# Kernel optimization log

Measured on AMD Instinct MI355X. Metric: run time of the kernel, lower is better.

The kernel has to match this reference:

```python
import jax, jax.numpy as jnp
import numpy as np

D = 256          # B == num_experts == hidden_dim == input_dim (required by the module's broadcasting)
NUM_HEADS = 4
LN_EPS = 1e-5


def _layer_norm(x, g, b):
    mu = jnp.mean(x, axis=-1, keepdims=True)
    var = jnp.mean(jnp.square(x - mu), axis=-1, keepdims=True)
    return (x - mu) * jax.lax.rsqrt(var + LN_EPS) * g + b


def setup_inputs() -> dict:
    key = jax.random.key(0)
    ks = jax.random.split(key, 12)
    B = E = H = IN = D
    s = 0.02
    return {
        "x": jax.random.normal(ks[0], (B, IN), jnp.float32),
        "task_embedding": jax.random.normal(ks[1], (B, H), jnp.float32),
        # stacked per-expert params: Linear(IN,H) -> LayerNorm(H) -> ReLU -> Linear(H,H)
        "W1": jax.random.normal(ks[2], (E, H, IN), jnp.float32) * s,
        "b1": jnp.zeros((E, H), jnp.float32),
        "ln1_g": jnp.ones((E, H), jnp.float32),
        "ln1_b": jnp.zeros((E, H), jnp.float32),
        "W2": jax.random.normal(ks[3], (E, H, H), jnp.float32) * s,
        "b2": jnp.zeros((E, H), jnp.float32),
        # MultiheadAttention in-projection (packed q,k,v). v/out_proj are dead code
        # in this forward (attn_output is discarded) but v slice kept for faithful shapes.
        "in_proj_w": jax.random.normal(ks[4], (3 * H, H), jnp.float32) * s,
        "in_proj_b": jnp.zeros((3 * H,), jnp.float32),
        # combine: Linear(H,H) -> LayerNorm(H) -> ReLU
        "cw": jax.random.normal(ks[5], (H, H), jnp.float32) * s,
        "cb": jnp.zeros((H,), jnp.float32),
        "cg": jnp.ones((H,), jnp.float32),
        "cbeta": jnp.zeros((H,), jnp.float32),
    }


def reference(x, task_embedding, W1, b1, ln1_g, ln1_b, W2, b2,
              in_proj_w, in_proj_b, cw, cb, cg, cbeta):
    B, H = x.shape
    hd = H // NUM_HEADS

    # ---- all experts on the same input (batched over expert axis) ----
    h = jnp.einsum('bi,eoi->beo', x, W1) + b1          # [B,E,H]
    h = _layer_norm(h, ln1_g, ln1_b)
    h = jax.nn.relu(h)
    eo = jnp.einsum('beh,eoh->beo', h, W2) + b2        # [B,E,H] expert_outputs

    # ---- attention gate (only attn_weights are used downstream) ----
    Wq, Wk = in_proj_w[:H], in_proj_w[H:2 * H]
    bq, bk = in_proj_b[:H], in_proj_b[H:2 * H]
    q = (task_embedding @ Wq.T + bq).reshape(B, NUM_HEADS, hd) / jnp.sqrt(jnp.float32(hd))
    k = (jnp.einsum('beh,oh->beo', eo, Wk) + bk).reshape(B, -1, NUM_HEADS, hd)
    scores = jnp.einsum('bnd,bend->bne', q, k)          # [B, heads, E]
    attn = jax.nn.softmax(scores, axis=-1)
    weights = jnp.mean(attn, axis=1)                    # [B, E] (avg over heads)

    # ---- faithful torch broadcasting of [B,E,H] * [1,B,E] (requires B==E==H) ----
    # combined[b,h] = sum_e eo[b,e,h] * weights[e,h]
    combined = jnp.einsum('beh,eh->bh', eo, weights)

    out = jax.nn.relu(_layer_norm(combined @ cw.T + cb, cg, cbeta))
    return out, weights[:, None, :], eo
```

## Files before the change

kernel.cpp:

```cpp
#include <hip/hip_runtime.h>

typedef _Float16 f16_t;
typedef f16_t f16x8 __attribute__((ext_vector_type(8)));
typedef float f32x4 __attribute__((ext_vector_type(4)));

#define MFMA16(a,b,c) __builtin_amdgcn_mfma_f32_16x16x32_f16(a,b,c,0,0,0)

__device__ __forceinline__ f16x8 cvt8h(float4 a, float4 b){
  f16x8 r;
  r[0]=(f16_t)a.x; r[1]=(f16_t)a.y; r[2]=(f16_t)a.z; r[3]=(f16_t)a.w;
  r[4]=(f16_t)b.x; r[5]=(f16_t)b.y; r[6]=(f16_t)b.z; r[7]=(f16_t)b.w;
  return r;
}

template<int NT>
__device__ __forceinline__ void stage_f16(const float* __restrict__ src,
                                          char* dst, int rows, int tid){
  const int nchunk = rows * 32;
  const float4* s4 = reinterpret_cast<const float4*>(src);
  for (int cid = tid; cid < nchunk; cid += NT){
    int r = cid >> 5, c = cid & 31;
    *reinterpret_cast<f16x8*>(dst + r*512 + ((c ^ (r&7))<<4)) = cvt8h(s4[cid*2], s4[cid*2+1]);
  }
}

__device__ __forceinline__ f16x8 ldsA(const char* buf, int row, int c16){
  return *reinterpret_cast<const f16x8*>(buf + row*512 + ((c16 ^ (row&7))<<4));
}

__device__ __forceinline__ void gemm_w16(f32x4 acc[4][2], const char* bufA,
    const f16_t* __restrict__ Wh, int n0, int lo16, int hi4){
  f16x8 bf[8][2];
  #pragma unroll
  for (int kb = 0; kb < 8; ++kb){
    #pragma unroll
    for (int nb = 0; nb < 2; ++nb)
      bf[kb][nb] = *reinterpret_cast<const f16x8*>(Wh + ((n0 + nb*16 + lo16)<<8) + kb*32 + hi4*8);
  }
  #pragma unroll
  for (int kb = 0; kb < 8; ++kb){
    #pragma unroll
    for (int mb = 0; mb < 4; ++mb){
      f16x8 af = ldsA(bufA, mb*16 + lo16, kb*4 + hi4);
      acc[mb][0] = MFMA16(af, bf[kb][0], acc[mb][0]);
      acc[mb][1] = MFMA16(af, bf[kb][1], acc[mb][1]);
    }
  }
}

__device__ __forceinline__ void gemm_w32(f32x4 acc[4][2], const char* bufA,
    const float* __restrict__ W, int n0, int lo16, int hi4){
  #pragma unroll
  for (int kb = 0; kb < 8; ++kb){
    f16x8 bf[2];
    #pragma unroll
    for (int nb = 0; nb < 2; ++nb){
      const float4* p = reinterpret_cast<const float4*>(W + ((n0 + nb*16 + lo16)<<8) + kb*32 + hi4*8);
      bf[nb] = cvt8h(p[0], p[1]);
    }
    #pragma unroll
    for (int mb = 0; mb < 4; ++mb){
      f16x8 af = ldsA(bufA, mb*16 + lo16, kb*4 + hi4);
      acc[mb][0] = MFMA16(af, bf[0], acc[mb][0]);
      acc[mb][1] = MFMA16(af, bf[1], acc[mb][1]);
    }
  }
}

__global__ __launch_bounds__(256)
void k0_cvt(const float* __restrict__ W1, const float* __restrict__ W2,
            const float* __restrict__ Wk, f16_t* __restrict__ w1h,
            f16_t* __restrict__ w2h, f16_t* __restrict__ wkh)
{
  const long long NG1 = 2097152, NG2 = 4194304, NGT = 4202496;
  for (long long gidx = (long long)blockIdx.x*256 + threadIdx.x; gidx < NGT;
       gidx += (long long)gridDim.x*256){
    const float4* s; f16_t* d; long long off;
    if (gidx < NG1){ s = (const float4*)W1; d = w1h; off = gidx; }
    else if (gidx < NG2){ s = (const float4*)W2; d = w2h; off = gidx - NG1; }
    else { s = (const float4*)Wk; d = wkh; off = gidx - NG2; }
    *reinterpret_cast<f16x8*>(d + off*8) = cvt8h(s[off*2], s[off*2+1]);
  }
}

template<int W16>
__global__ __launch_bounds__(512, 4)
void k2_fused(const float* __restrict__ x, const void* __restrict__ W1v,
              const float* __restrict__ b1, const float* __restrict__ g1,
              const float* __restrict__ bb1, const void* __restrict__ W2v,
              const float* __restrict__ b2, const void* __restrict__ Wkv,
              const float* __restrict__ ipb, const float* __restrict__ q,
              float* __restrict__ eo_out, float* __restrict__ scores)
{
  __shared__ __align__(16) char lds[37376];
  char* bufA = lds;
  float* red = (float*)(lds + 32768);
  float* st  = (float*)(lds + 36864);

  const int l = blockIdx.x;
  const int e    = (l & 7) * 32 + (l >> 5);
  const int b0   = ((l >> 3) & 3) * 64;
  const int tid = threadIdx.x;
  const int lane = tid & 63, wid = tid >> 6;
  const int lo16 = lane & 15, hi4 = lane >> 4;
  const int n0 = wid * 32;

  stage_f16<512>(x + b0*256, bufA, 64, tid);
  __syncthreads();

  f32x4 acc[4][2];
  #pragma unroll
  for (int mb=0;mb<4;++mb){
    #pragma unroll
    for (int nb=0;nb<2;++nb) acc[mb][nb] = (f32x4)0.0f;
  }

  if (W16) gemm_w16(acc, bufA, (const f16_t*)W1v + e*65536, n0, lo16, hi4);
  else     gemm_w32(acc, bufA, (const float*)W1v + e*65536, n0, lo16, hi4);

  float b1v[2], g1v[2], bbv[2];
  #pragma unroll
  for (int nb=0;nb<2;++nb){
    int c = n0 + nb*16 + lo16;
    b1v[nb] = b1[e*256 + c];
    g1v[nb] = g1[e*256 + c];
    bbv[nb] = bb1[e*256 + c];
  }
  #pragma unroll
  for (int mb=0;mb<4;++mb){
    #pragma unroll
    for (int nb=0;nb<2;++nb){
      #pragma unroll
      for (int r=0;r<4;++r) acc[mb][nb][r] += b1v[nb];
    }
  }

  #pragma unroll
  for (int mb=0;mb<4;++mb){
    #pragma unroll
    for (int r=0;r<4;++r){
      float s=0.f, ss=0.f;
      #pragma unroll
      for (int nb=0;nb<2;++nb){ float v = acc[mb][nb][r]; s += v; ss += v*v; }
      #pragma unroll
      for (int m=1;m<16;m<<=1){ s += __shfl_xor(s, m, 64); ss += __shfl_xor(ss, m, 64); }
      if (lo16 == 0){
        int row = mb*16 + hi4*4 + r;
        red[row*16 + wid]     = s;
        red[row*16 + 8 + wid] = ss;
      }
    }
  }
  __syncthreads();
  if (tid < 64){
    float s  = 0.f, ss = 0.f;
    #pragma unroll
    for (int i=0;i<8;++i){ s += red[tid*16 + i]; ss += red[tid*16 + 8 + i]; }
    float mu = s * (1.f/256.f);
    float var = ss * (1.f/256.f) - mu*mu;
    st[tid*2]   = mu;
    st[tid*2+1] = rsqrtf(var + 1e-5f);
  }
  __syncthreads();

  #pragma unroll
  for (int mb=0;mb<4;++mb){
    #pragma unroll
    for (int r=0;r<4;++r){
      int row = mb*16 + hi4*4 + r;
      float mu = st[row*2], rs = st[row*2+1];
      #pragma unroll
      for (int nb=0;nb<2;++nb){
        int c = n0 + nb*16 + lo16;
        float v = (acc[mb][nb][r] - mu) * rs * g1v[nb] + bbv[nb];
        v = fmaxf(v, 0.f);
        int off = row*512 + (((c>>3) ^ (row&7))<<4) + (c&7)*2;
        *reinterpret_cast<f16_t*>(bufA + off) = (f16_t)v;
      }
    }
  }
  __syncthreads();

  #pragma unroll
  for (int mb=0;mb<4;++mb){
    #pragma unroll
    for (int nb=0;nb<2;++nb) acc[mb][nb] = (f32x4)0.0f;
  }
  if (W16) gemm_w16(acc, bufA, (const f16_t*)W2v + e*65536, n0, lo16, hi4);
  else     gemm_w32(acc, bufA, (const float*)W2v + e*65536, n0, lo16, hi4);

  float b2v[2];
  #pragma unroll
  for (int nb=0;nb<2;++nb) b2v[nb] = b2[e*256 + n0 + nb*16 + lo16];

  __syncthreads();

  #pragma unroll
  for (int mb=0;mb<4;++mb){
    #pragma unroll
    for (int r=0;r<4;++r){
      int row = mb*16 + hi4*4 + r;
      int b = b0 + row;
      #pragma unroll
      for (int nb=0;nb<2;++nb){
        int c = n0 + nb*16 + lo16;
        float v = acc[mb][nb][r] + b2v[nb];
        eo_out[(b*256 + e)*256 + c] = v;
        int off = row*512 + (((c>>3) ^ (row&7))<<4) + (c&7)*2;
        *reinterpret_cast<f16_t*>(bufA + off) = (f16_t)v;
      }
    }
  }
  __syncthreads();

  #pragma unroll
  for (int mb=0;mb<4;++mb){
    #pragma unroll
    for (int nb=0;nb<2;++nb) acc[mb][nb] = (f32x4)0.0f;
  }
  if (W16) gemm_w16(acc, bufA, (const f16_t*)Wkv, n0, lo16, hi4);
  else     gemm_w32(acc, bufA, (const float*)Wkv, n0, lo16, hi4);

  float bkv[2];
  #pragma unroll
  for (int nb=0;nb<2;++nb) bkv[nb] = ipb[256 + n0 + nb*16 + lo16];

  #pragma unroll
  for (int mb=0;mb<4;++mb){
    #pragma unroll
    for (int r=0;r<4;++r){
      int row = mb*16 + hi4*4 + r;
      int b = b0 + row;
      float p = 0.f;
      #pragma unroll
      for (int nb=0;nb<2;++nb){
        int c = n0 + nb*16 + lo16;
        p += q[b*256 + c] * (acc[mb][nb][r] + bkv[nb]);
      }
      #pragma unroll
      for (int m=1;m<16;m<<=1) p += __shfl_xor(p, m, 64);
      if (lo16 == 0) red[row*16 + wid] = p;
    }
  }
  __syncthreads();
  if (tid < 256){
    int row = tid >> 2, hd = tid & 3;
    float sc = red[row*16 + hd*2] + red[row*16 + hd*2 + 1];
    scores[((b0 + row)*4 + hd)*256 + e] = sc;
  }
}

__global__ __launch_bounds__(512, 4)
void k_mini(const float* __restrict__ A, const float* __restrict__ W,
            const float* __restrict__ bias, float scale, int do_ln,
            const float* __restrict__ g, const float* __restrict__ bb,
            int do_relu, float* __restrict__ out)
{
  __shared__ __align__(16) char lds[18688];
  char* bufA = lds;
  float* red = (float*)(lds + 16384);
  float* st  = (float*)(lds + 18432);

  const int b0 = blockIdx.x * 32;
  const int tid = threadIdx.x;
  const int lane = tid & 63, wid = tid >> 6;
  const int lo16 = lane & 15, hi4 = lane >> 4;
  const int n0 = wid * 32;

  stage_f16<512>(A + b0*256, bufA, 32, tid);
  __syncthreads();

  f32x4 acc[2][2];
  #pragma unroll
  for (int mb=0;mb<2;++mb){
    #pragma unroll
    for (int nb=0;nb<2;++nb) acc[mb][nb] = (f32x4)0.0f;
  }
  #pragma unroll
  for (int kb = 0; kb < 8; ++kb){
    f16x8 bf[2];
    #pragma unroll
    for (int nb = 0; nb < 2; ++nb){
      const float4* p = reinterpret_cast<const float4*>(W + ((n0 + nb*16 + lo16)<<8) + kb*32 + hi4*8);
      bf[nb] = cvt8h(p[0], p[1]);
    }
    #pragma unroll
    for (int mb = 0; mb < 2; ++mb){
      f16x8 af = ldsA(bufA, mb*16 + lo16, kb*4 + hi4);
      acc[mb][0] = MFMA16(af, bf[0], acc[mb][0]);
      acc[mb][1] = MFMA16(af, bf[1], acc[mb][1]);
    }
  }

  float bv[2], gv[2], bbv[2];
  #pragma unroll
  for (int nb=0;nb<2;++nb){
    int c = n0 + nb*16 + lo16;
    bv[nb]  = bias[c];
    gv[nb]  = do_ln ? g[c]  : 1.f;
    bbv[nb] = do_ln ? bb[c] : 0.f;
  }
  #pragma unroll
  for (int mb=0;mb<2;++mb){
    #pragma unroll
    for (int nb=0;nb<2;++nb){
      #pragma unroll
      for (int r=0;r<4;++r) acc[mb][nb][r] = (acc[mb][nb][r] + bv[nb]) * scale;
    }
  }

  if (do_ln){
    #pragma unroll
    for (int mb=0;mb<2;++mb){
      #pragma unroll
      for (int r=0;r<4;++r){
        float s=0.f, ss=0.f;
        #pragma unroll
        for (int nb=0;nb<2;++nb){ float v = acc[mb][nb][r]; s += v; ss += v*v; }
        #pragma unroll
        for (int m=1;m<16;m<<=1){ s += __shfl_xor(s, m, 64); ss += __shfl_xor(ss, m, 64); }
        if (lo16 == 0){
          int row = mb*16 + hi4*4 + r;
          red[row*16 + wid]     = s;
          red[row*16 + 8 + wid] = ss;
        }
      }
    }
    __syncthreads();
    if (tid < 32){
      float s = 0.f, ss = 0.f;
      #pragma unroll
      for (int i=0;i<8;++i){ s += red[tid*16 + i]; ss += red[tid*16 + 8 + i]; }
      float mu = s * (1.f/256.f);
      float var = ss * (1.f/256.f) - mu*mu;
      st[tid*2]   = mu;
      st[tid*2+1] = rsqrtf(var + 1e-5f);
    }
    __syncthreads();
  }

  #pragma unroll
  for (int mb=0;mb<2;++mb){
    #pragma unroll
    for (int r=0;r<4;++r){
      int row = mb*16 + hi4*4 + r;
      float mu = 0.f, rs = 1.f;
      if (do_ln){ mu = st[row*2]; rs = st[row*2+1]; }
      #pragma unroll
      for (int nb=0;nb<2;++nb){
        int c = n0 + nb*16 + lo16;
        float v = acc[mb][nb][r];
        if (do_ln) v = (v - mu) * rs * gv[nb] + bbv[nb];
        if (do_relu) v = fmaxf(v, 0.f);
        out[(b0 + row)*256 + c] = v;
      }
    }
  }
}

__global__ __launch_bounds__(256)
void k3_softmax(const float* __restrict__ scores, float* __restrict__ wts)
{
  const int b = blockIdx.x, t = threadIdx.x;
  const int wid = t >> 6, lane = t & 63;
  __shared__ float r4[4];
  float sc[4];
  #pragma unroll
  for (int n=0;n<4;++n) sc[n] = scores[(b*4 + n)*256 + t];
  float wsum = 0.f;
  for (int n=0;n<4;++n){
    float m = sc[n];
    #pragma unroll
    for (int k=1;k<64;k<<=1) m = fmaxf(m, __shfl_xor(m, k, 64));
    if (lane == 0) r4[wid] = m;
    __syncthreads();
    m = fmaxf(fmaxf(r4[0], r4[1]), fmaxf(r4[2], r4[3]));
    __syncthreads();
    float ex = __expf(sc[n] - m);
    float s = ex;
    #pragma unroll
    for (int k=1;k<64;k<<=1) s += __shfl_xor(s, k, 64);
    if (lane == 0) r4[wid] = s;
    __syncthreads();
    s = r4[0] + r4[1] + r4[2] + r4[3];
    __syncthreads();
    wsum += ex / s;
  }
  wts[b*256 + t] = wsum * 0.25f;
}

__global__ __launch_bounds__(1024)
void k4a_combined(const float* __restrict__ eo, const float* __restrict__ wts,
                  float* __restrict__ cmb)
{
  __shared__ float part[1024];
  const int b = blockIdx.x, t = threadIdx.x;
  const int c = t >> 8, h = t & 255;
  const float* p = eo + b*65536 + h;
  float s = 0.f;
  #pragma unroll 8
  for (int i = 0; i < 64; ++i){
    int e2 = c*64 + i;
    s += p[e2*256] * wts[e2*256 + h];
  }
  part[t] = s;
  __syncthreads();
  if (t < 256) cmb[b*256 + t] = part[t] + part[t+256] + part[t+512] + part[t+768];
}

extern "C" void kernel_launch(void* const* d_in, const int* in_sizes, int n_in,
                              void* d_out, int out_size, void* d_ws, size_t ws_size,
                              hipStream_t stream)
{
  const float* x    = (const float*)d_in[0];
  const float* te   = (const float*)d_in[1];
  const float* W1   = (const float*)d_in[2];
  const float* b1   = (const float*)d_in[3];
  const float* g1   = (const float*)d_in[4];
  const float* bb1  = (const float*)d_in[5];
  const float* W2   = (const float*)d_in[6];
  const float* b2   = (const float*)d_in[7];
  const float* ipw  = (const float*)d_in[8];
  const float* ipb  = (const float*)d_in[9];
  const float* cw   = (const float*)d_in[10];
  const float* cb   = (const float*)d_in[11];
  const float* cg   = (const float*)d_in[12];
  const float* cbt  = (const float*)d_in[13];

  float* out    = (float*)d_out;
  float* wts    = out + 65536;
  float* eo     = out + 131072;

  const size_t F16_BYTES = 2ull*(16777216ull*2 + 65536);
  const size_t NEED = F16_BYTES + 4ull*(65536 + 262144 + 65536);
  const bool f16w = ws_size >= NEED;

  f16_t* w1h = (f16_t*)d_ws;
  f16_t* w2h = w1h + 16777216;
  f16_t* wkh = w2h + 16777216;
  float* fbase = f16w ? (float*)((char*)d_ws + F16_BYTES) : (float*)d_ws;
  float* q      = fbase;
  float* scores = q + 65536;
  float* cmb    = scores + 262144;

  k_mini<<<8, 512, 0, stream>>>(te, ipw, ipb, 0.125f, 0, nullptr, nullptr, 0, q);

  if (f16w){
    k0_cvt<<<2048, 256, 0, stream>>>(W1, W2, ipw + 65536, w1h, w2h, wkh);
    k2_fused<1><<<1024, 512, 0, stream>>>(x, w1h, b1, g1, bb1, w2h, b2,
                                          wkh, ipb, q, eo, scores);
  } else {
    k2_fused<0><<<1024, 512, 0, stream>>>(x, W1, b1, g1, bb1, W2, b2,
                                          ipw + 65536, ipb, q, eo, scores);
  }

  k3_softmax<<<256, 256, 0, stream>>>(scores, wts);
  k4a_combined<<<256, 1024, 0, stream>>>(eo, wts, cmb);
  k_mini<<<8, 512, 0, stream>>>(cmb, cw, cb, 1.0f, 1, cg, cbt, 1, out);
}
```

Baseline: 148.3 us.

## Pipeline weight tiles through LDS with async global_load_lds double buffering

Measured after the change: 143.6 us. 1.03x faster.

```diff
diff --git a/kernel.cpp b/kernel.cpp
--- a/kernel.cpp
+++ b/kernel.cpp
@@ -5,6 +5,14 @@
 typedef float f32x4 __attribute__((ext_vector_type(4)));
 
 #define MFMA16(a,b,c) __builtin_amdgcn_mfma_f32_16x16x32_f16(a,b,c,0,0,0)
+#define VM0 asm volatile("s_waitcnt vmcnt(0)" ::: "memory")
+#define VM2 asm volatile("s_waitcnt vmcnt(2)" ::: "memory")
+
+__device__ __forceinline__ void cp16(const void* g, void* l){
+  __builtin_amdgcn_global_load_lds(
+      (const __attribute__((address_space(1))) void*)g,
+      (__attribute__((address_space(3))) void*)l, 16, 0, 0);
+}
 
 __device__ __forceinline__ f16x8 cvt8h(float4 a, float4 b){
   f16x8 r;
@@ -28,23 +36,29 @@
   return *reinterpret_cast<const f16x8*>(buf + row*512 + ((c16 ^ (row&7))<<4));
 }
 
-__device__ __forceinline__ void gemm_w16(f32x4 acc[4][2], const char* bufA,
-    const f16_t* __restrict__ Wh, int n0, int lo16, int hi4){
-  f16x8 bf[8][2];
+__device__ __forceinline__ void issue_tile(const f16_t* wsrc, int kb, char* wt, int lane){
+  const f16_t* s = wsrc + kb*32;
+  char* d = wt + (kb&1)*2048 + lane*16;
+  cp16(s, d);
+  cp16(s + 16*256, d + 1024);
+}
+
+__device__ __forceinline__ void gemm_pipe(f32x4 acc[4][2], const char* bufA,
+    const f16_t* wsrc, char* wt, int lane, int lo16, int hi4){
   #pragma unroll
   for (int kb = 0; kb < 8; ++kb){
-    #pragma unroll
-    for (int nb = 0; nb < 2; ++nb)
-      bf[kb][nb] = *reinterpret_cast<const f16x8*>(Wh + ((n0 + nb*16 + lo16)<<8) + kb*32 + hi4*8);
-  }
-  #pragma unroll
-  for (int kb = 0; kb < 8; ++kb){
+    if (kb < 7) { VM2; } else { VM0; }
+    const char* ws = wt + (kb&1)*2048 + lo16*64 + hi4*16;
+    f16x8 bf0 = *reinterpret_cast<const f16x8*>(ws);
+    f16x8 bf1 = *reinterpret_cast<const f16x8*>(ws + 1024);
     #pragma unroll
     for (int mb = 0; mb < 4; ++mb){
       f16x8 af = ldsA(bufA, mb*16 + lo16, kb*4 + hi4);
-      acc[mb][0] = MFMA16(af, bf[kb][0], acc[mb][0]);
-      acc[mb][1] = MFMA16(af, bf[kb][1], acc[mb][1]);
-    }
+      acc[mb][0] = MFMA16(af, bf0, acc[mb][0]);
+      acc[mb][1] = MFMA16(af, bf1, acc[mb][1]);
+    }
+    __builtin_amdgcn_sched_barrier(0);
+    if (kb + 2 < 8) issue_tile(wsrc, kb + 2, wt, lane);
   }
 }
 
@@ -92,10 +106,11 @@
               const float* __restrict__ ipb, const float* __restrict__ q,
               float* __restrict__ eo_out, float* __restrict__ scores)
 {
-  __shared__ __align__(16) char lds[37376];
+  __shared__ __align__(16) char lds[70144];
   char* bufA = lds;
   float* red = (float*)(lds + 32768);
   float* st  = (float*)(lds + 36864);
+  char* wpipe = lds + 37376;
 
   const int l = blockIdx.x;
   const int e    = (l & 7) * 32 + (l >> 5);
@@ -104,6 +119,17 @@
   const int lane = tid & 63, wid = tid >> 6;
   const int lo16 = lane & 15, hi4 = lane >> 4;
   const int n0 = wid * 32;
+  char* wt = wpipe + wid*4096;
+
+  const int r_in = lane >> 2, c_in = (lane & 3) * 8;
+  const f16_t* src1 = nullptr; const f16_t* src2 = nullptr; const f16_t* srcK = nullptr;
+  if (W16){
+    src1 = (const f16_t*)W1v + e*65536 + (n0 + r_in)*256 + c_in;
+    src2 = (const f16_t*)W2v + e*65536 + (n0 + r_in)*256 + c_in;
+    srcK = (const f16_t*)Wkv +           (n0 + r_in)*256 + c_in;
+    issue_tile(src1, 0, wt, lane);
+    issue_tile(src1, 1, wt, lane);
+  }
 
   stage_f16<512>(x + b0*256, bufA, 64, tid);
   __syncthreads();
@@ -115,8 +141,13 @@
     for (int nb=0;nb<2;++nb) acc[mb][nb] = (f32x4)0.0f;
   }
 
-  if (W16) gemm_w16(acc, bufA, (const f16_t*)W1v + e*65536, n0, lo16, hi4);
+  if (W16) gemm_pipe(acc, bufA, src1, wt, lane, lo16, hi4);
   else     gemm_w32(acc, bufA, (const float*)W1v + e*65536, n0, lo16, hi4);
+
+  if (W16){
+    issue_tile(src2, 0, wt, lane);
+    issue_tile(src2, 1, wt, lane);
+  }
 
   float b1v[2], g1v[2], bbv[2];
   #pragma unroll
@@ -186,7 +217,7 @@
     #pragma unroll
     for (int nb=0;nb<2;++nb) acc[mb][nb] = (f32x4)0.0f;
   }
-  if (W16) gemm_w16(acc, bufA, (const f16_t*)W2v + e*65536, n0, lo16, hi4);
+  if (W16) gemm_pipe(acc, bufA, src2, wt, lane, lo16, hi4);
   else     gemm_w32(acc, bufA, (const float*)W2v + e*65536, n0, lo16, hi4);
 
   float b2v[2];
@@ -194,6 +225,11 @@
   for (int nb=0;nb<2;++nb) b2v[nb] = b2[e*256 + n0 + nb*16 + lo16];
 
   __syncthreads();
+
+  if (W16){
+    issue_tile(srcK, 0, wt, lane);
+    issue_tile(srcK, 1, wt, lane);
+  }
 
   #pragma unroll
   for (int mb=0;mb<4;++mb){
@@ -218,7 +254,7 @@
     #pragma unroll
     for (int nb=0;nb<2;++nb) acc[mb][nb] = (f32x4)0.0f;
   }
-  if (W16) gemm_w16(acc, bufA, (const f16_t*)Wkv, n0, lo16, hi4);
+  if (W16) gemm_pipe(acc, bufA, srcK, wt, lane, lo16, hi4);
   else     gemm_w32(acc, bufA, (const float*)Wkv, n0, lo16, hi4);
 
   float bkv[2];
```
